# Performance work log

Hardware: AMD Instinct MI355X
Metric: run time of the kernel (lower is better)

## Reference

```python
import jax, jax.numpy as jnp
import numpy as np

ALPHA = 0.7
NUM_HEADS = 12
NUM_KV_HEADS = 6
HEAD_DIM = 64
ROPE_BASE = 10000.0


def ternary_quantize(w):
    thr = ALPHA * jnp.mean(jnp.abs(w))
    return jnp.sign(w) * (jnp.abs(w) >= thr).astype(w.dtype)


def bitlinear(x, w):
    # forward: F.linear(x, ternary(w)) * mean(|w|)
    scale = jnp.mean(jnp.abs(w))
    qw = ternary_quantize(w)
    return (x @ qw.T) * scale


def rope_tables(seq_len, dim, dtype):
    inv_freq = 1.0 / (ROPE_BASE ** (jnp.arange(0, dim, 2, dtype=jnp.float32) / dim))
    t = jnp.arange(seq_len, dtype=jnp.float32)
    freqs = jnp.outer(t, inv_freq)            # [S, dim/2]
    emb = jnp.concatenate([freqs, freqs], -1)  # [S, dim]
    return jnp.cos(emb).astype(dtype), jnp.sin(emb).astype(dtype)


def rotate_half(x):
    x1, x2 = jnp.split(x, 2, axis=-1)
    return jnp.concatenate([-x2, x1], axis=-1)


def setup_inputs() -> dict:
    key = jax.random.key(0)
    ks = jax.random.split(key, 5)
    B, S, H = 2, 2048, 768
    return {
        "hidden_states": jax.random.normal(ks[0], (B, S, H), jnp.float32),
        "Wq": jax.random.normal(ks[1], (768, 768), jnp.float32) * 0.02,
        "Wk": jax.random.normal(ks[2], (384, 768), jnp.float32) * 0.02,
        "Wv": jax.random.normal(ks[3], (384, 768), jnp.float32) * 0.02,
        "Wo": jax.random.normal(ks[4], (768, 768), jnp.float32) * 0.02,
    }


def reference(hidden_states, Wq, Wk, Wv, Wo):
    B, S, H = hidden_states.shape
    nh, nkv, hd = NUM_HEADS, NUM_KV_HEADS, HEAD_DIM
    groups = nh // nkv

    q = bitlinear(hidden_states, Wq).reshape(B, S, nh, hd).transpose(0, 2, 1, 3)
    k = bitlinear(hidden_states, Wk).reshape(B, S, nkv, hd).transpose(0, 2, 1, 3)
    v = bitlinear(hidden_states, Wv).reshape(B, S, nkv, hd).transpose(0, 2, 1, 3)

    cos, sin = rope_tables(S, hd, hidden_states.dtype)  # [S, hd]
    cos = cos[None, None]  # [1,1,S,hd]
    sin = sin[None, None]
    q = q * cos + rotate_half(q) * sin
    k = k * cos + rotate_half(k) * sin

    # GQA: expand kv heads to full head count
    k = jnp.repeat(k, groups, axis=1)  # [B, nh, S, hd]
    v = jnp.repeat(v, groups, axis=1)

    scale = 1.0 / jnp.sqrt(jnp.asarray(hd, hidden_states.dtype))
    scores = jnp.einsum("bhsd,bhtd->bhst", q, k) * scale
    attn = jax.nn.softmax(scores, axis=-1)
    out = jnp.einsum("bhst,bhtd->bhsd", attn, v)
    out = out.transpose(0, 2, 1, 3).reshape(B, S, H)
    return bitlinear(out, Wo)
```

## Files before the change

kernel.cpp:

```cpp
#include <hip/hip_runtime.h>
#include <cmath>

typedef unsigned short u16;
typedef unsigned int u32;
typedef __bf16 bf16x2 __attribute__((ext_vector_type(2)));
typedef __bf16 bf16x8 __attribute__((ext_vector_type(8)));
typedef float f32x16 __attribute__((ext_vector_type(16)));

#define NQ (768*768)
#define NK (384*768)

__device__ __forceinline__ u16 f2bf(float f) {
  u32 u = __float_as_uint(f);
  u32 r = (u + 0x7FFFu + ((u >> 16) & 1u)) >> 16;
  return (u16)r;
}
__device__ __forceinline__ u32 packbf(float a, float b) {
#if __has_builtin(__builtin_amdgcn_cvt_pk_bf16_f32)
  bf16x2 v = __builtin_amdgcn_cvt_pk_bf16_f32(a, b);
  u32 r; __builtin_memcpy(&r, &v, 4); return r;
#else
  return (u32)f2bf(a) | ((u32)f2bf(b) << 16);
#endif
}
__device__ __forceinline__ float fexp2(float x) {
#if __has_builtin(__builtin_amdgcn_exp2f)
  return __builtin_amdgcn_exp2f(x);
#else
  return exp2f(x);
#endif
}
__device__ __forceinline__ bf16x8 ldfrag(const u16* p) { bf16x8 v; __builtin_memcpy(&v, p, 16); return v; }
__device__ __forceinline__ f32x16 mfma32_(bf16x8 a, bf16x8 b, f32x16 c) {
  return __builtin_amdgcn_mfma_f32_32x32x16_bf16(a, b, c, 0, 0, 0);
}

__device__ __forceinline__ int fidx(int r, int k) {
  return (r >> 5) * 24576 + (k >> 4) * 512 + ((r & 31) + 32 * ((k >> 3) & 1)) * 8 + (k & 7);
}
__device__ __forceinline__ int kidx(int b6kvh, int s, int d) {
  return b6kvh * 131072 + (s >> 5) * 2048 + (d >> 4) * 512 +
         ((s & 31) + 32 * ((d >> 3) & 1)) * 8 + (d & 7);
}
__device__ __forceinline__ int qidx(int b, int s, int h, int d) {
  return ((b * 64 + (s >> 5)) * 12 + h) * 2048 + (d >> 4) * 512 +
         ((s & 31) + 32 * ((d >> 3) & 1)) * 8 + (d & 7);
}
__device__ __forceinline__ int vidx(int b6kvh, int d, int p) {
  return b6kvh * 131072 + (p >> 6) * 4096 + (d >> 5) * 2048 + ((p >> 4) & 3) * 512 +
         ((d & 31) + 32 * ((p >> 3) & 1)) * 8 + (p & 7);
}

__global__ __launch_bounds__(256) void abssum_kernel(const float* __restrict__ wq, const float* __restrict__ wk,
                                                     const float* __restrict__ wv, const float* __restrict__ wo,
                                                     float* __restrict__ sums) {
  int which = blockIdx.y;
  const float* w = (which == 0) ? wq : (which == 1) ? wk : (which == 2) ? wv : wo;
  int n4 = ((which == 0 || which == 3) ? NQ : NK) >> 2;
  const float4* w4 = (const float4*)w;
  float s = 0.f;
  for (int i = blockIdx.x * blockDim.x + threadIdx.x; i < n4; i += gridDim.x * blockDim.x) {
    float4 v = w4[i];
    s += fabsf(v.x) + fabsf(v.y) + fabsf(v.z) + fabsf(v.w);
  }
  for (int off = 32; off; off >>= 1) s += __shfl_down(s, off);
  __shared__ float ls[4];
  if ((threadIdx.x & 63) == 0) ls[threadIdx.x >> 6] = s;
  __syncthreads();
  if (threadIdx.x == 0) atomicAdd(&sums[which], ls[0] + ls[1] + ls[2] + ls[3]);
}

__global__ __launch_bounds__(256) void prep_kernel(const float* __restrict__ wq, const float* __restrict__ wk,
                                                   const float* __restrict__ wv, const float* __restrict__ wo,
                                                   const float* __restrict__ sums, const float* __restrict__ x,
                                                   u16* __restrict__ qw, u16* __restrict__ woq,
                                                   u16* __restrict__ xb) {
  int i = blockIdx.x * blockDim.x + threadIdx.x;
  if (i < 221184) {
    int n = i / 96, k8 = i - n * 96;
    const float* src; float th; u16* dst; int nd;
    if (n < 768)       { src = wq + n * 768;          th = 0.7f * sums[0] * (1.f / NQ); dst = qw;  nd = n; }
    else if (n < 1152) { src = wk + (n - 768) * 768;  th = 0.7f * sums[1] * (1.f / NK); dst = qw;  nd = n; }
    else if (n < 1536) { src = wv + (n - 1152) * 768; th = 0.7f * sums[2] * (1.f / NK); dst = qw;  nd = n; }
    else               { src = wo + (n - 1536) * 768; th = 0.7f * sums[3] * (1.f / NQ); dst = woq; nd = n - 1536; }
    const float4* sp = (const float4*)(src + k8 * 8);
    float4 v0 = sp[0], v1 = sp[1];
    float e[8] = {v0.x, v0.y, v0.z, v0.w, v1.x, v1.y, v1.z, v1.w};
    u16 o[8];
#pragma unroll
    for (int j = 0; j < 8; j++)
      o[j] = f2bf((fabsf(e[j]) >= th) ? ((e[j] > 0.f) ? 1.f : -1.f) : 0.f);
    __builtin_memcpy(dst + fidx(nd, k8 * 8), o, 16);
  } else {
    int j = i - 221184;
    int m = j / 96, k8 = j - m * 96;
    const float4* xp = (const float4*)(x + m * 768 + k8 * 8);
    float4 v0 = xp[0], v1 = xp[1];
    u16 o[8] = { f2bf(v0.x), f2bf(v0.y), f2bf(v0.z), f2bf(v0.w),
                 f2bf(v1.x), f2bf(v1.y), f2bf(v1.z), f2bf(v1.w) };
    __builtin_memcpy(xb + fidx(m, k8 * 8), o, 16);
  }
}

__global__ __launch_bounds__(256, 3) void gemm_qkv_kernel(const u16* __restrict__ xb, const u16* __restrict__ qw,
                                                          const float* __restrict__ sums,
                                                          u16* __restrict__ qb, u16* __restrict__ kb,
                                                          u16* __restrict__ vT) {
  int tn = blockIdx.x, tm = blockIdx.y;
  int t = threadIdx.x, lane = t & 63, w = t >> 6, c = lane & 31, g2 = lane >> 5;
  int wm = w & 1, wn = w >> 1;
  const u16* abase = xb + (tm * 2 + wm) * 24576 + lane * 8;
  const u16* bbase0 = qw + (tn * 4 + wn * 2) * 24576 + lane * 8;
  const u16* bbase1 = bbase0 + 24576;
  f32x16 acc[2]; acc[0] = (f32x16)0.f; acc[1] = (f32x16)0.f;
  for (int kk = 0; kk < 48; kk += 4) {
#pragma unroll
    for (int ks = 0; ks < 4; ks++) {
      bf16x8 af = ldfrag(abase + (kk + ks) * 512);
      bf16x8 b0 = ldfrag(bbase0 + (kk + ks) * 512);
      bf16x8 b1 = ldfrag(bbase1 + (kk + ks) * 512);
      acc[0] = mfma32_(af, b0, acc[0]);
      acc[1] = mfma32_(af, b1, acc[1]);
    }
  }
  float sq = sums[0] * (1.f / NQ) * 0.180336880111120f;
  float sk = sums[1] * (1.f / NK);
  float sv = sums[2] * (1.f / NK);
  int mb = tm * 64 + wm * 32 + 4 * g2;
  if (tn < 9) {
    float sc = (tn < 6) ? sq : sk;
    int head = (tn < 6) ? (tn * 2 + wn) : ((tn - 6) * 2 + wn);
    float f = fexp2((float)c * -0.41524101186092029f);
#pragma unroll
    for (int r = 0; r < 16; r++) {
      int m = mb + (r & 3) + 8 * (r >> 2);
      int bb = m >> 11, s = m & 2047;
      float sn, cs; sincosf((float)s * f, &sn, &cs);
      float x1 = acc[0][r] * sc, x2 = acc[1][r] * sc;
      u16 y1 = f2bf(x1 * cs - x2 * sn);
      u16 y2 = f2bf(x2 * cs + x1 * sn);
      if (tn < 6) {
        qb[qidx(bb, s, head, c)]      = y1;
        qb[qidx(bb, s, head, c + 32)] = y2;
      } else {
        kb[kidx(bb * 6 + head, s, c)]      = y1;
        kb[kidx(bb * 6 + head, s, c + 32)] = y2;
      }
    }
  } else {
    int kvh = (tn - 9) * 2 + wn;
#pragma unroll
    for (int nb = 0; nb < 2; nb++)
#pragma unroll
      for (int r = 0; r < 16; r++) {
        int m = mb + (r & 3) + 8 * (r >> 2);
        int bb = m >> 11, s = m & 2047;
        int sp = (s & ~12) | ((s & 4) << 1) | ((s & 8) >> 1);
        vT[vidx(bb * 6 + kvh, nb * 32 + c, sp)] = f2bf(acc[nb][r] * sv);
      }
  }
}

__global__ __launch_bounds__(256, 3) void attn_kernel(const u16* __restrict__ qb, const u16* __restrict__ kb,
                                                      const u16* __restrict__ vT, u16* __restrict__ ab) {
  __shared__ float Obuf[4][32][66];
  __shared__ float Lbuf[4][32];
  int bk = blockIdx.x, qt = blockIdx.y;
  int b = bk / 6, kvh = bk % 6;
  int t = threadIdx.x, lane = t & 63, w = t >> 6, c = lane & 31, g2 = lane >> 5;
  int qn = w & 1, kh = w >> 1;

  const u16* qbase = qb + ((b * 64 + qt) * 12 + kvh * 2 + qn) * 2048;
  bf16x8 qf[4];
#pragma unroll
  for (int ks = 0; ks < 4; ks++) qf[ks] = ldfrag(qbase + ks * 512 + lane * 8);

  u32 onesw = 0x3F803F80u;
  bf16x8 ones;
  { u32 tmp[4] = {onesw, onesw, onesw, onesw}; __builtin_memcpy(&ones, tmp, 16); }

  f32x16 fz = (f32x16)0.f;
  f32x16 O[2] = {fz, fz};
  f32x16 Lacc = fz;

  const u16* Kb = kb + bk * 131072;
  const u16* Vb = vT + bk * 131072;

  for (int it = 0; it < 32; it++) {
    int kb32 = kh * 32 + it;
    const u16* kt = Kb + kb32 * 2048;
    const u16* vt = Vb + (kb32 >> 1) * 4096 + (kb32 & 1) * 1024;
    bf16x8 kf[4];
#pragma unroll
    for (int ks = 0; ks < 4; ks++) kf[ks] = ldfrag(kt + ks * 512 + lane * 8);
    bf16x8 vf[2][2];
#pragma unroll
    for (int dn = 0; dn < 2; dn++)
#pragma unroll
      for (int ksv = 0; ksv < 2; ksv++)
        vf[dn][ksv] = ldfrag(vt + dn * 2048 + ksv * 512 + lane * 8);
    f32x16 S = fz;
#pragma unroll
    for (int ks = 0; ks < 4; ks++) S = mfma32_(kf[ks], qf[ks], S);
    float e[16];
#pragma unroll
    for (int r = 0; r < 16; r++) e[r] = fexp2(S[r]);
    u32 P[8];
#pragma unroll
    for (int j = 0; j < 8; j++) P[j] = packbf(e[2 * j], e[2 * j + 1]);
    bf16x8 PA[2];
    __builtin_memcpy(&PA[0], &P[0], 16);
    __builtin_memcpy(&PA[1], &P[4], 16);
#pragma unroll
    for (int ksv = 0; ksv < 2; ksv++) {
      O[0] = mfma32_(PA[ksv], vf[0][ksv], O[0]);
      O[1] = mfma32_(PA[ksv], vf[1][ksv], O[1]);
      Lacc = mfma32_(PA[ksv], ones, Lacc);
    }
  }
  if (c == 0) {
#pragma unroll
    for (int r = 0; r < 16; r++) Lbuf[w][(r & 3) + 8 * (r >> 2) + 4 * g2] = Lacc[r];
  }
#pragma unroll
  for (int dn = 0; dn < 2; dn++)
#pragma unroll
    for (int r = 0; r < 16; r++)
      Obuf[w][(r & 3) + 8 * (r >> 2) + 4 * g2][dn * 32 + c] = O[dn][r];
  __syncthreads();
  {
    int hn = t >> 7, qq = (t >> 2) & 31, dc = (t & 3) * 16;
    float l = Lbuf[hn][qq] + Lbuf[hn + 2][qq];
    float inv = 1.f / l;
    u16 o[16];
#pragma unroll
    for (int j = 0; j < 16; j++)
      o[j] = f2bf((Obuf[hn][qq][dc + j] + Obuf[hn + 2][qq][dc + j]) * inv);
    int h = kvh * 2 + hn;
    int mg = b * 64 + qt;
    u16* dst = ab + mg * 24576 + ((h * 64 + dc) >> 4) * 512 + qq * 8;
    __builtin_memcpy(dst, o, 16);
    __builtin_memcpy(dst + 256, o + 8, 16);
  }
}

__global__ __launch_bounds__(256, 3) void gemm_out_kernel(const u16* __restrict__ ab, const u16* __restrict__ woq,
                                                          const float* __restrict__ sums, float* __restrict__ out) {
  int tn = blockIdx.x, tm = blockIdx.y;
  int t = threadIdx.x, lane = t & 63, w = t >> 6, c = lane & 31, g2 = lane >> 5;
  int wm = w & 1, wn = w >> 1;
  const u16* abase = ab + (tm * 2 + wm) * 24576 + lane * 8;
  const u16* bbase = woq + (tn * 2 + wn) * 24576 + lane * 8;
  f32x16 acc = (f32x16)0.f;
  for (int kk = 0; kk < 48; kk += 4) {
#pragma unroll
    for (int ks = 0; ks < 4; ks++) {
      bf16x8 af = ldfrag(abase + (kk + ks) * 512);
      bf16x8 bf = ldfrag(bbase + (kk + ks) * 512);
      acc = mfma32_(af, bf, acc);
    }
  }
  float so = sums[3] * (1.f / NQ);
  int mb = tm * 64 + wm * 32 + 4 * g2;
#pragma unroll
  for (int r = 0; r < 16; r++) {
    int m = mb + (r & 3) + 8 * (r >> 2);
    out[m * 768 + tn * 64 + wn * 32 + c] = acc[r] * so;
  }
}

extern "C" void kernel_launch(void* const* d_in, const int* in_sizes, int n_in,
                              void* d_out, int out_size, void* d_ws, size_t ws_size,
                              hipStream_t stream) {
  const float* x  = (const float*)d_in[0];
  const float* wq = (const float*)d_in[1];
  const float* wk = (const float*)d_in[2];
  const float* wv = (const float*)d_in[3];
  const float* wo = (const float*)d_in[4];
  float* out = (float*)d_out;
  char* ws = (char*)d_ws;

  float* sums = (float*)ws;
  u16* qw  = (u16*)(ws + 256);
  u16* woq = (u16*)(ws + 2359552);
  u16* xb  = (u16*)(ws + 3539200);
  u16* qb  = (u16*)(ws + 9830656);
  u16* kb  = (u16*)(ws + 16122112);
  u16* vT  = (u16*)(ws + 19267840);
  u16* ab  = (u16*)(ws + 22413568);

  hipMemsetAsync(sums, 0, 16, stream);
  dim3 blk(256);
  abssum_kernel<<<dim3(64, 4), blk, 0, stream>>>(wq, wk, wv, wo, sums);
  prep_kernel<<<dim3(2400), blk, 0, stream>>>(wq, wk, wv, wo, sums, x, qw, woq, xb);
  gemm_qkv_kernel<<<dim3(12, 64), blk, 0, stream>>>(xb, qw, sums, qb, kb, vT);
  attn_kernel<<<dim3(12, 64), blk, 0, stream>>>(qb, kb, vT, ab);
  gemm_out_kernel<<<dim3(12, 64), blk, 0, stream>>>(ab, woq, sums, out);
}
```

Baseline: 158.9 us.

## Double-buffer fragment loads in GEMMs and attention, precompute RoPE table, VALU row sums

Both GEMM kernels and the attention loop now double-buffer their fragment loads, issuing the next K-chunk's loads before the current chunk's MFMAs so memory latency overlaps with compute. The per-element sincosf in the QKV epilogue is replaced by lookups into a cos/sin table that the prep kernel computes once per launch. Attention row sums are now accumulated with VALU adds plus a cross-lane shuffle instead of an extra MFMA against a ones vector. The cost is higher register pressure under the (256,3) launch bounds and an extra table read in the epilogue.

After: 156.2 us. No clear change (-1.7%).

```diff
diff --git a/kernel.cpp b/kernel.cpp
--- a/kernel.cpp
+++ b/kernel.cpp
@@ -74,7 +74,7 @@
                                                    const float* __restrict__ wv, const float* __restrict__ wo,
                                                    const float* __restrict__ sums, const float* __restrict__ x,
                                                    u16* __restrict__ qw, u16* __restrict__ woq,
-                                                   u16* __restrict__ xb) {
+                                                   u16* __restrict__ xb, float2* __restrict__ rt) {
   int i = blockIdx.x * blockDim.x + threadIdx.x;
   if (i < 221184) {
     int n = i / 96, k8 = i - n * 96;
@@ -91,7 +91,7 @@
     for (int j = 0; j < 8; j++)
       o[j] = f2bf((fabsf(e[j]) >= th) ? ((e[j] > 0.f) ? 1.f : -1.f) : 0.f);
     __builtin_memcpy(dst + fidx(nd, k8 * 8), o, 16);
-  } else {
+  } else if (i < 614400) {
     int j = i - 221184;
     int m = j / 96, k8 = j - m * 96;
     const float4* xp = (const float4*)(x + m * 768 + k8 * 8);
@@ -99,11 +99,18 @@
     u16 o[8] = { f2bf(v0.x), f2bf(v0.y), f2bf(v0.z), f2bf(v0.w),
                  f2bf(v1.x), f2bf(v1.y), f2bf(v1.z), f2bf(v1.w) };
     __builtin_memcpy(xb + fidx(m, k8 * 8), o, 16);
+  } else {
+    int j = i - 614400;
+    int s = j >> 5, c = j & 31;
+    float f = exp2f((float)c * -0.41524101186092029f);
+    float sn, cs; sincosf((float)s * f, &sn, &cs);
+    rt[j] = make_float2(cs, sn);
   }
 }
 
 __global__ __launch_bounds__(256, 3) void gemm_qkv_kernel(const u16* __restrict__ xb, const u16* __restrict__ qw,
                                                           const float* __restrict__ sums,
+                                                          const float2* __restrict__ rt,
                                                           u16* __restrict__ qb, u16* __restrict__ kb,
                                                           u16* __restrict__ vT) {
   int tn = blockIdx.x, tm = blockIdx.y;
@@ -113,14 +120,38 @@
   const u16* bbase0 = qw + (tn * 4 + wn * 2) * 24576 + lane * 8;
   const u16* bbase1 = bbase0 + 24576;
   f32x16 acc[2]; acc[0] = (f32x16)0.f; acc[1] = (f32x16)0.f;
-  for (int kk = 0; kk < 48; kk += 4) {
+  bf16x8 aA[4], c0A[4], c1A[4], aB[4], c0B[4], c1B[4];
+#pragma unroll
+  for (int ks = 0; ks < 4; ks++) {
+    aA[ks]  = ldfrag(abase + ks * 512);
+    c0A[ks] = ldfrag(bbase0 + ks * 512);
+    c1A[ks] = ldfrag(bbase1 + ks * 512);
+  }
+#pragma unroll
+  for (int kk = 0; kk < 48; kk += 8) {
 #pragma unroll
     for (int ks = 0; ks < 4; ks++) {
-      bf16x8 af = ldfrag(abase + (kk + ks) * 512);
-      bf16x8 b0 = ldfrag(bbase0 + (kk + ks) * 512);
-      bf16x8 b1 = ldfrag(bbase1 + (kk + ks) * 512);
-      acc[0] = mfma32_(af, b0, acc[0]);
-      acc[1] = mfma32_(af, b1, acc[1]);
+      aB[ks]  = ldfrag(abase + (kk + 4 + ks) * 512);
+      c0B[ks] = ldfrag(bbase0 + (kk + 4 + ks) * 512);
+      c1B[ks] = ldfrag(bbase1 + (kk + 4 + ks) * 512);
+    }
+#pragma unroll
+    for (int ks = 0; ks < 4; ks++) {
+      acc[0] = mfma32_(aA[ks], c0A[ks], acc[0]);
+      acc[1] = mfma32_(aA[ks], c1A[ks], acc[1]);
+    }
+    if (kk + 8 < 48) {
+#pragma unroll
+      for (int ks = 0; ks < 4; ks++) {
+        aA[ks]  = ldfrag(abase + (kk + 8 + ks) * 512);
+        c0A[ks] = ldfrag(bbase0 + (kk + 8 + ks) * 512);
+        c1A[ks] = ldfrag(bbase1 + (kk + 8 + ks) * 512);
+      }
+    }
+#pragma unroll
+    for (int ks = 0; ks < 4; ks++) {
+      acc[0] = mfma32_(aB[ks], c0B[ks], acc[0]);
+      acc[1] = mfma32_(aB[ks], c1B[ks], acc[1]);
     }
   }
   float sq = sums[0] * (1.f / NQ) * 0.180336880111120f;
@@ -130,15 +161,15 @@
   if (tn < 9) {
     float sc = (tn < 6) ? sq : sk;
     int head = (tn < 6) ? (tn * 2 + wn) : ((tn - 6) * 2 + wn);
-    float f = fexp2((float)c * -0.41524101186092029f);
+    const float2* rp = rt + c;
 #pragma unroll
     for (int r = 0; r < 16; r++) {
       int m = mb + (r & 3) + 8 * (r >> 2);
       int bb = m >> 11, s = m & 2047;
-      float sn, cs; sincosf((float)s * f, &sn, &cs);
+      float2 cs2 = rp[s << 5];
       float x1 = acc[0][r] * sc, x2 = acc[1][r] * sc;
-      u16 y1 = f2bf(x1 * cs - x2 * sn);
-      u16 y2 = f2bf(x2 * cs + x1 * sn);
+      u16 y1 = f2bf(x1 * cs2.x - x2 * cs2.y);
+      u16 y2 = f2bf(x2 * cs2.x + x1 * cs2.y);
       if (tn < 6) {
         qb[qidx(bb, s, head, c)]      = y1;
         qb[qidx(bb, s, head, c + 32)] = y2;
@@ -159,6 +190,39 @@
         vT[vidx(bb * 6 + kvh, nb * 32 + c, sp)] = f2bf(acc[nb][r] * sv);
       }
   }
+}
+
+__device__ __forceinline__ void load_k4(bf16x8 (&kf)[4], const u16* Kb, int grp, int lane) {
+  const u16* kt = Kb + grp * 2048 + lane * 8;
+#pragma unroll
+  for (int ks = 0; ks < 4; ks++) kf[ks] = ldfrag(kt + ks * 512);
+}
+__device__ __forceinline__ void load_v4(bf16x8 (&vf)[2][2], const u16* Vb, int grp, int lane) {
+  const u16* vt = Vb + (grp >> 1) * 4096 + (grp & 1) * 1024 + lane * 8;
+  vf[0][0] = ldfrag(vt);
+  vf[0][1] = ldfrag(vt + 512);
+  vf[1][0] = ldfrag(vt + 2048);
+  vf[1][1] = ldfrag(vt + 2048 + 512);
+}
+__device__ __forceinline__ void attn_step(const bf16x8 (&kf)[4], const bf16x8 (&vf)[2][2],
+                                          const bf16x8 (&qf)[4], f32x16 (&O)[2], float& lsum) {
+  f32x16 S = (f32x16)0.f;
+#pragma unroll
+  for (int ks = 0; ks < 4; ks++) S = mfma32_(kf[ks], qf[ks], S);
+#pragma unroll
+  for (int r = 0; r < 16; r++) S[r] = fexp2(S[r]);
+  lsum += (((S[0] + S[1]) + (S[2] + S[3])) + ((S[4] + S[5]) + (S[6] + S[7])))
+        + (((S[8] + S[9]) + (S[10] + S[11])) + ((S[12] + S[13]) + (S[14] + S[15])));
+  u32 P[8];
+#pragma unroll
+  for (int j = 0; j < 8; j++) P[j] = packbf(S[2 * j], S[2 * j + 1]);
+  bf16x8 PA0, PA1;
+  __builtin_memcpy(&PA0, &P[0], 16);
+  __builtin_memcpy(&PA1, &P[4], 16);
+  O[0] = mfma32_(PA0, vf[0][0], O[0]);
+  O[1] = mfma32_(PA0, vf[1][0], O[1]);
+  O[0] = mfma32_(PA1, vf[0][1], O[0]);
+  O[1] = mfma32_(PA1, vf[1][1], O[1]);
 }
 
 __global__ __launch_bounds__(256, 3) void attn_kernel(const u16* __restrict__ qb, const u16* __restrict__ kb,
@@ -175,53 +239,30 @@
 #pragma unroll
   for (int ks = 0; ks < 4; ks++) qf[ks] = ldfrag(qbase + ks * 512 + lane * 8);
 
-  u32 onesw = 0x3F803F80u;
-  bf16x8 ones;
-  { u32 tmp[4] = {onesw, onesw, onesw, onesw}; __builtin_memcpy(&ones, tmp, 16); }
-
   f32x16 fz = (f32x16)0.f;
   f32x16 O[2] = {fz, fz};
-  f32x16 Lacc = fz;
+  float lsum = 0.f;
 
   const u16* Kb = kb + bk * 131072;
   const u16* Vb = vT + bk * 131072;
 
-  for (int it = 0; it < 32; it++) {
-    int kb32 = kh * 32 + it;
-    const u16* kt = Kb + kb32 * 2048;
-    const u16* vt = Vb + (kb32 >> 1) * 4096 + (kb32 & 1) * 1024;
-    bf16x8 kf[4];
-#pragma unroll
-    for (int ks = 0; ks < 4; ks++) kf[ks] = ldfrag(kt + ks * 512 + lane * 8);
-    bf16x8 vf[2][2];
-#pragma unroll
-    for (int dn = 0; dn < 2; dn++)
-#pragma unroll
-      for (int ksv = 0; ksv < 2; ksv++)
-        vf[dn][ksv] = ldfrag(vt + dn * 2048 + ksv * 512 + lane * 8);
-    f32x16 S = fz;
-#pragma unroll
-    for (int ks = 0; ks < 4; ks++) S = mfma32_(kf[ks], qf[ks], S);
-    float e[16];
-#pragma unroll
-    for (int r = 0; r < 16; r++) e[r] = fexp2(S[r]);
-    u32 P[8];
-#pragma unroll
-    for (int j = 0; j < 8; j++) P[j] = packbf(e[2 * j], e[2 * j + 1]);
-    bf16x8 PA[2];
-    __builtin_memcpy(&PA[0], &P[0], 16);
-    __builtin_memcpy(&PA[1], &P[4], 16);
-#pragma unroll
-    for (int ksv = 0; ksv < 2; ksv++) {
-      O[0] = mfma32_(PA[ksv], vf[0][ksv], O[0]);
-      O[1] = mfma32_(PA[ksv], vf[1][ksv], O[1]);
-      Lacc = mfma32_(PA[ksv], ones, Lacc);
-    }
-  }
-  if (c == 0) {
-#pragma unroll
-    for (int r = 0; r < 16; r++) Lbuf[w][(r & 3) + 8 * (r >> 2) + 4 * g2] = Lacc[r];
-  }
+  bf16x8 kfA[4], kfB[4], vfA[2][2], vfB[2][2];
+  int g = kh * 32;
+  load_k4(kfA, Kb, g, lane);
+  load_v4(vfA, Vb, g, lane);
+  for (int it2 = 0; it2 < 16; ++it2) {
+    load_k4(kfB, Kb, g + 1, lane);
+    load_v4(vfB, Vb, g + 1, lane);
+    attn_step(kfA, vfA, qf, O, lsum);
+    if (it2 < 15) {
+      load_k4(kfA, Kb, g + 2, lane);
+      load_v4(vfA, Vb, g + 2, lane);
+    }
+    attn_step(kfB, vfB, qf, O, lsum);
+    g += 2;
+  }
+  float ltot = lsum + __shfl_xor(lsum, 32);
+  if (g2 == 0) Lbuf[w][c] = ltot;
 #pragma unroll
   for (int dn = 0; dn < 2; dn++)
 #pragma unroll
@@ -252,13 +293,30 @@
   const u16* abase = ab + (tm * 2 + wm) * 24576 + lane * 8;
   const u16* bbase = woq + (tn * 2 + wn) * 24576 + lane * 8;
   f32x16 acc = (f32x16)0.f;
-  for (int kk = 0; kk < 48; kk += 4) {
+  bf16x8 aA[4], bA[4], aB[4], bB[4];
+#pragma unroll
+  for (int ks = 0; ks < 4; ks++) {
+    aA[ks] = ldfrag(abase + ks * 512);
+    bA[ks] = ldfrag(bbase + ks * 512);
+  }
+#pragma unroll
+  for (int kk = 0; kk < 48; kk += 8) {
 #pragma unroll
     for (int ks = 0; ks < 4; ks++) {
-      bf16x8 af = ldfrag(abase + (kk + ks) * 512);
-      bf16x8 bf = ldfrag(bbase + (kk + ks) * 512);
-      acc = mfma32_(af, bf, acc);
-    }
+      aB[ks] = ldfrag(abase + (kk + 4 + ks) * 512);
+      bB[ks] = ldfrag(bbase + (kk + 4 + ks) * 512);
+    }
+#pragma unroll
+    for (int ks = 0; ks < 4; ks++) acc = mfma32_(aA[ks], bA[ks], acc);
+    if (kk + 8 < 48) {
+#pragma unroll
+      for (int ks = 0; ks < 4; ks++) {
+        aA[ks] = ldfrag(abase + (kk + 8 + ks) * 512);
+        bA[ks] = ldfrag(bbase + (kk + 8 + ks) * 512);
+      }
+    }
+#pragma unroll
+    for (int ks = 0; ks < 4; ks++) acc = mfma32_(aB[ks], bB[ks], acc);
   }
   float so = sums[3] * (1.f / NQ);
   int mb = tm * 64 + wm * 32 + 4 * g2;
@@ -288,12 +346,13 @@
   u16* kb  = (u16*)(ws + 16122112);
   u16* vT  = (u16*)(ws + 19267840);
   u16* ab  = (u16*)(ws + 22413568);
+  float2* rt = (float2*)(ws + 28705024);
 
   hipMemsetAsync(sums, 0, 16, stream);
   dim3 blk(256);
   abssum_kernel<<<dim3(64, 4), blk, 0, stream>>>(wq, wk, wv, wo, sums);
-  prep_kernel<<<dim3(2400), blk, 0, stream>>>(wq, wk, wv, wo, sums, x, qw, woq, xb);
-  gemm_qkv_kernel<<<dim3(12, 64), blk, 0, stream>>>(xb, qw, sums, qb, kb, vT);
+  prep_kernel<<<dim3(2656), blk, 0, stream>>>(wq, wk, wv, wo, sums, x, qw, woq, xb, rt);
+  gemm_qkv_kernel<<<dim3(12, 64), blk, 0, stream>>>(xb, qw, sums, rt, qb, kb, vT);
   attn_kernel<<<dim3(12, 64), blk, 0, stream>>>(qb, kb, vT, ab);
   gemm_out_kernel<<<dim3(12, 64), blk, 0, stream>>>(ab, woq, sums, out);
 }
```
